# Optimization experiments

Hardware: AMD Instinct MI355X
Metric: run time of the kernel (lower is better)

Reference implementation:

```python
import jax, jax.numpy as jnp
import numpy as np

N = 50000   # nodes
D = 128     # hidden_dim == in_dim
H = 4       # heads
C = 32      # hidden_dim // heads
L = 3       # message_layers
ET = 640000 # temporal edges
EH = 320000 # host edges


def layer_norm(x, g, b, eps=1e-5):
    m = x.mean(-1, keepdims=True)
    v = ((x - m) ** 2).mean(-1, keepdims=True)
    return (x - m) / jnp.sqrt(v + eps) * g + b


def transformer_conv(h, src, dst, e_emb, Wq, bq, Wk, bk, Wv, bv, We, Ws, bs):
    # PyG TransformerConv, concat=True, root_weight=True, beta=False
    n = h.shape[0]
    q = (h @ Wq + bq).reshape(n, H, C)
    k = (h @ Wk + bk).reshape(n, H, C)
    v = (h @ Wv + bv).reshape(n, H, C)
    ee = (e_emb @ We).reshape(-1, H, C)          # lin_edge has no bias
    kj = k[src] + ee                              # [E,H,C]
    a = (q[dst] * kj).sum(-1) / np.sqrt(C)        # [E,H]
    amax = jax.ops.segment_max(a, dst, num_segments=n)
    amax = jnp.where(jnp.isfinite(amax), amax, 0.0)
    ex = jnp.exp(a - amax[dst])
    den = jax.ops.segment_sum(ex, dst, num_segments=n)
    alpha = ex / (den[dst] + 1e-16)               # segment softmax over in-edges of dst
    msg = (v[src] + ee) * alpha[..., None]        # [E,H,C]
    out = jax.ops.segment_sum(msg, dst, num_segments=n).reshape(n, H * C)
    return out + h @ Ws + bs                      # root/skip connection


def mlp_head(h, W1, b1, g, bt, W2, b2):
    z = jax.nn.silu(h @ W1 + b1)
    z = layer_norm(z, g, bt)
    return z @ W2 + b2


def setup_inputs() -> dict:
    key = jax.random.key(0)
    ks = iter(jax.random.split(key, 80))
    nrm = lambda shape: jax.random.normal(next(ks), shape, jnp.float32) * 0.05
    inp = {}
    inp['x'] = jax.random.normal(next(ks), (N, D), jnp.float32)
    inp['edge_index_temporal'] = jax.random.randint(next(ks), (2, ET), 0, N)
    inp['edge_index_host'] = jax.random.randint(next(ks), (2, EH), 0, N)
    inp['edge_attr_temporal'] = jax.random.uniform(next(ks), (ET, 1), jnp.float32)
    inp['edge_attr_host'] = jax.random.normal(next(ks), (EH, 3), jnp.float32)
    # edge encoders
    inp['W_tedge'] = nrm((1, 4)); inp['b_tedge'] = jnp.zeros(4)
    inp['W_hedge'] = nrm((3, 4)); inp['b_hedge'] = jnp.zeros(4)
    # stacked conv params [L, ...] for temporal (_t) and host (_h) convs
    for s in ('t', 'h'):
        inp[f'Wq_{s}'] = nrm((L, D, D)); inp[f'bq_{s}'] = jnp.zeros((L, D))
        inp[f'Wk_{s}'] = nrm((L, D, D)); inp[f'bk_{s}'] = jnp.zeros((L, D))
        inp[f'Wv_{s}'] = nrm((L, D, D)); inp[f'bv_{s}'] = jnp.zeros((L, D))
        inp[f'We_{s}'] = nrm((L, 4, D))
        inp[f'Ws_{s}'] = nrm((L, D, D)); inp[f'bs_{s}'] = jnp.zeros((L, D))
    inp['norm_g'] = jnp.ones((L, D)); inp['norm_b'] = jnp.zeros((L, D))
    inp['fg'] = jnp.ones(D); inp['fb'] = jnp.zeros(D)
    inp['dW1'] = nrm((D, D)); inp['db1'] = jnp.zeros(D)
    inp['dg'] = jnp.ones(D); inp['dbt'] = jnp.zeros(D)
    inp['dW2'] = nrm((D, 3)); inp['db2'] = jnp.zeros(3)
    inp['sW1'] = nrm((D, D)); inp['sb1'] = jnp.zeros(D)
    inp['sg'] = jnp.ones(D); inp['sbt'] = jnp.zeros(D)
    inp['sW2'] = nrm((D, 3)); inp['sb2'] = jnp.zeros(3)
    return inp


def reference(x, edge_index_temporal, edge_index_host, edge_attr_temporal, edge_attr_host,
              W_tedge, b_tedge, W_hedge, b_hedge,
              Wq_t, bq_t, Wk_t, bk_t, Wv_t, bv_t, We_t, Ws_t, bs_t,
              Wq_h, bq_h, Wk_h, bk_h, Wv_h, bv_h, We_h, Ws_h, bs_h,
              norm_g, norm_b, fg, fb,
              dW1, db1, dg, dbt, dW2, db2,
              sW1, sb1, sg, sbt, sW2, sb2):
    te = edge_attr_temporal @ W_tedge + b_tedge   # [ET, edge_dim]
    he = edge_attr_host @ W_hedge + b_hedge       # [EH, edge_dim]
    st, dt_ = edge_index_temporal[0], edge_index_temporal[1]
    sh, dh = edge_index_host[0], edge_index_host[1]
    h = x
    for l in range(L):
        t_out = transformer_conv(h, st, dt_, te, Wq_t[l], bq_t[l], Wk_t[l], bk_t[l],
                                 Wv_t[l], bv_t[l], We_t[l], Ws_t[l], bs_t[l])
        h_out = transformer_conv(h, sh, dh, he, Wq_h[l], bq_h[l], Wk_h[l], bk_h[l],
                                 Wv_h[l], bv_h[l], We_h[l], Ws_h[l], bs_h[l])
        combined = jax.nn.silu(layer_norm(t_out + h_out, norm_g[l], norm_b[l]))
        h = h + combined  # residual (shapes match since in_dim == hidden_dim)
    h = layer_norm(h, fg, fb)
    drift = mlp_head(h, dW1, db1, dg, dbt, dW2, db2)
    diff = mlp_head(h, sW1, sb1, sg, sbt, sW2, sb2)
    return drift, diff
```

## Files before the change

### kernel.cpp

```cpp
#include <hip/hip_runtime.h>
#include <math.h>

#define NN 50000
#define DD 128
#define ET_N 640000
#define EH_N 320000
#define NL 3

static inline int cdiv(int a, int b){ return (a+b-1)/b; }

typedef __attribute__((ext_vector_type(8))) short short8;
typedef __attribute__((ext_vector_type(4))) float f32x4;

__device__ float   g_h [(size_t)NN*DD];
__device__ unsigned short g_hb[(size_t)NN*DD];
__device__ unsigned short g_Wb[(size_t)NL*8*DD*DD];
__device__ float   g_Q [2][(size_t)NN*DD];
__device__ float   g_S [2][(size_t)NN*DD];
__device__ ushort2 g_KV[2][(size_t)NN*DD];
__device__ float   g_to[(size_t)NN*DD];
__device__ float   g_ho[(size_t)NN*DD];
__device__ int     g_cnt[2][NN];
__device__ int     g_cur[2][NN];
__device__ int     g_rs [2][NN+1];
__device__ int     g_srcc[2][ET_N];
__device__ float4  g_ee  [2][ET_N];

__device__ inline unsigned short f2bf(float f){
  unsigned u = __float_as_uint(f);
  unsigned r = (u + 0x7fffu + ((u>>16)&1u)) >> 16;
  return (unsigned short)r;
}
__device__ inline float bf2f(unsigned short s){
  return __uint_as_float(((unsigned)s)<<16);
}

__global__ void k_copy_h(const float* __restrict__ x){
  int i = blockIdx.x*256 + threadIdx.x;
  if (i < NN*DD/4){
    float4 v = reinterpret_cast<const float4*>(x)[i];
    reinterpret_cast<float4*>(g_h)[i] = v;
    ushort4 b; b.x=f2bf(v.x); b.y=f2bf(v.y); b.z=f2bf(v.z); b.w=f2bf(v.w);
    reinterpret_cast<ushort4*>(g_hb)[i] = b;
  }
}

__global__ void k_zero_cnt(){
  int i = blockIdx.x*256 + threadIdx.x;
  if (i < NN) g_cnt[blockIdx.y][i] = 0;
}

struct WPtrs { const float* W[24]; };
__global__ __launch_bounds__(256) void k_cvtw(WPtrs wp){
  int mat = blockIdx.y;
  const float* W = wp.W[mat];
  int e = blockIdx.x*256 + threadIdx.x;
  int n = e >> 7, k = e & 127;
  g_Wb[(size_t)mat*DD*DD + e] = f2bf(W[k*DD+n]);
}

__global__ void k_hist(const int* __restrict__ dstT, const int* __restrict__ dstH){
  int which = blockIdx.y;
  int E = which ? EH_N : ET_N;
  const int* dst = which ? dstH : dstT;
  int e = blockIdx.x*256+threadIdx.x;
  if (e<E) atomicAdd(&g_cnt[which][dst[e]], 1);
}

__global__ __launch_bounds__(1024) void k_scan(){
  int which = blockIdx.y;
  int* row_start = g_rs[which];
  const int* cnt = g_cnt[which];
  int* cur = g_cur[which];
  __shared__ int buf[1024];
  int tid = threadIdx.x;
  const int n = NN;
  int chunk = (n + 1023) >> 10;
  int start = tid*chunk; if (start>n) start=n;
  int end = start+chunk; if (end>n) end=n;
  int lsum=0;
  for (int i=start;i<end;++i) lsum += cnt[i];
  buf[tid]=lsum;
  __syncthreads();
  for (int off=1; off<1024; off<<=1){
    int t = (tid>=off)? buf[tid-off]:0;
    __syncthreads();
    buf[tid] += t;
    __syncthreads();
  }
  int run = buf[tid]-lsum;
  for (int i=start;i<end;++i){ row_start[i]=run; cur[i]=run; run += cnt[i]; }
  if (tid==1023) row_start[n]=run;
}

__global__ void k_scatter(const int* __restrict__ eit, const int* __restrict__ eih,
                          const float* __restrict__ attrT, const float* __restrict__ attrH,
                          const float* __restrict__ Wt, const float* __restrict__ bt4,
                          const float* __restrict__ Wh, const float* __restrict__ bh4){
  int which = blockIdx.y;
  int e = blockIdx.x*256+threadIdx.x;
  if (which==0){
    if (e>=ET_N) return;
    int src = eit[e], dst = eit[ET_N+e];
    int p = atomicAdd(&g_cur[0][dst],1);
    g_srcc[0][p]=src;
    float a = attrT[e];
    g_ee[0][p] = make_float4(a*Wt[0]+bt4[0], a*Wt[1]+bt4[1], a*Wt[2]+bt4[2], a*Wt[3]+bt4[3]);
  } else {
    if (e>=EH_N) return;
    int src = eih[e], dst = eih[EH_N+e];
    int p = atomicAdd(&g_cur[1][dst],1);
    g_srcc[1][p]=src;
    float a0=attrH[e*3+0], a1=attrH[e*3+1], a2=attrH[e*3+2];
    float4 v;
    v.x = a0*Wh[0]+a1*Wh[4]+a2*Wh[8]+bh4[0];
    v.y = a0*Wh[1]+a1*Wh[5]+a2*Wh[9]+bh4[1];
    v.z = a0*Wh[2]+a1*Wh[6]+a2*Wh[10]+bh4[2];
    v.w = a0*Wh[3]+a1*Wh[7]+a2*Wh[11]+bh4[3];
    g_ee[1][p] = v;
  }
}

struct BiasP { const float* b[8]; };

__global__ __launch_bounds__(256) void k_gemm_mfma(int l, BiasP bp){
  __shared__ unsigned short lA[64*DD];
  __shared__ unsigned short lB[DD*DD];
  int y = blockIdx.y;
  int conv = y/3, kind = y%3;
  int setbase = l*8 + conv*4;
  const unsigned short* Wm0 = &g_Wb[(size_t)(setbase + (kind==0?0:(kind==1?1:3)))*DD*DD];
  const unsigned short* Wm1 = &g_Wb[(size_t)(setbase+2)*DD*DD];
  int tid = threadIdx.x;
  int m0 = blockIdx.x*64;

#pragma unroll
  for (int p=0;p<4;++p){
    int c = tid + p*256;
    int row = c >> 4, col16 = c & 15;
    int grow = m0 + row;
    uint4 v = make_uint4(0,0,0,0);
    if (grow < NN) v = *reinterpret_cast<const uint4*>(&g_hb[(size_t)grow*DD + col16*8]);
    int off = (row*256 + col16*16) ^ ((row&7)<<4);
    *reinterpret_cast<uint4*>((char*)lA + off) = v;
  }
#pragma unroll
  for (int p=0;p<8;++p){
    int c = tid + p*256;
    int row = c >> 4, col16 = c & 15;
    uint4 v = *reinterpret_cast<const uint4*>(&Wm0[(size_t)row*DD + col16*8]);
    int off = (row*256 + col16*16) ^ ((row&7)<<4);
    *reinterpret_cast<uint4*>((char*)lB + off) = v;
  }
  __syncthreads();

  int wave = tid >> 6, lane = tid & 63;
  int lrow = lane & 15, kg = lane >> 4;
  int n0w = wave*32;

  short8 a[4][4];
#pragma unroll
  for (int kk=0;kk<4;++kk){
    int kbyte = kk*64 + kg*16;
#pragma unroll
    for (int mi=0;mi<4;++mi){
      int row = mi*16 + lrow;
      int off = (row*256 + kbyte) ^ ((row&7)<<4);
      a[kk][mi] = *reinterpret_cast<const short8*>((char*)lA + off);
    }
  }

  f32x4 acc[4][2];
#pragma unroll
  for (int mi=0;mi<4;++mi)
#pragma unroll
    for (int ni=0;ni<2;++ni) acc[mi][ni] = (f32x4){0.f,0.f,0.f,0.f};

#pragma unroll
  for (int kk=0;kk<4;++kk){
    int kbyte = kk*64 + kg*16;
    short8 b[2];
#pragma unroll
    for (int ni=0;ni<2;++ni){
      int n = n0w + ni*16 + lrow;
      int off = (n*256 + kbyte) ^ ((n&7)<<4);
      b[ni] = *reinterpret_cast<const short8*>((char*)lB + off);
    }
#pragma unroll
    for (int mi=0;mi<4;++mi)
#pragma unroll
      for (int ni=0;ni<2;++ni)
        acc[mi][ni] = __builtin_amdgcn_mfma_f32_16x16x32_bf16(a[kk][mi], b[ni], acc[mi][ni], 0,0,0);
  }

  f32x4 acc2[4][2];
  if (kind==1){
    __syncthreads();
#pragma unroll
    for (int p=0;p<8;++p){
      int c = tid + p*256;
      int row = c >> 4, col16 = c & 15;
      uint4 v = *reinterpret_cast<const uint4*>(&Wm1[(size_t)row*DD + col16*8]);
      int off = (row*256 + col16*16) ^ ((row&7)<<4);
      *reinterpret_cast<uint4*>((char*)lB + off) = v;
    }
    __syncthreads();
#pragma unroll
    for (int mi=0;mi<4;++mi)
#pragma unroll
      for (int ni=0;ni<2;++ni) acc2[mi][ni] = (f32x4){0.f,0.f,0.f,0.f};
#pragma unroll
    for (int kk=0;kk<4;++kk){
      int kbyte = kk*64 + kg*16;
      short8 b[2];
#pragma unroll
      for (int ni=0;ni<2;++ni){
        int n = n0w + ni*16 + lrow;
        int off = (n*256 + kbyte) ^ ((n&7)<<4);
        b[ni] = *reinterpret_cast<const short8*>((char*)lB + off);
      }
#pragma unroll
      for (int mi=0;mi<4;++mi)
#pragma unroll
        for (int ni=0;ni<2;++ni)
          acc2[mi][ni] = __builtin_amdgcn_mfma_f32_16x16x32_bf16(a[kk][mi], b[ni], acc2[mi][ni], 0,0,0);
    }
  }

  const float* bias0 = bp.b[conv*4 + (kind==0?0:(kind==1?1:3))];
  const float* bias1 = bp.b[conv*4 + 2];
#pragma unroll
  for (int ni=0;ni<2;++ni){
    int col = n0w + ni*16 + lrow;
    float bs0 = bias0[col];
    float bs1 = (kind==1) ? bias1[col] : 0.f;
#pragma unroll
    for (int mi=0;mi<4;++mi){
#pragma unroll
      for (int r=0;r<4;++r){
        int row = m0 + mi*16 + kg*4 + r;
        if (row >= NN) continue;
        size_t o = (size_t)row*DD + col;
        if (kind==1){
          ushort2 kv;
          kv.x = f2bf(acc[mi][ni][r]  + bs0);
          kv.y = f2bf(acc2[mi][ni][r] + bs1);
          g_KV[conv][o] = kv;
        } else {
          float* op = (kind==0) ? g_Q[conv] : g_S[conv];
          op[o] = acc[mi][ni][r] + bs0;
        }
      }
    }
  }
}

__global__ __launch_bounds__(128) void k_agg(const float* __restrict__ WeT,
                                             const float* __restrict__ WeH){
  int conv = blockIdx.y;
  int i = blockIdx.x;
  int d = threadIdx.x;
  const float* We = conv ? WeH : WeT;
  float w0=We[d], w1=We[DD+d], w2=We[2*DD+d], w3=We[3*DD+d];
  float qd = g_Q[conv][(size_t)i*DD+d];
  const int*     srcc = g_srcc[conv];
  const float4*  ee   = g_ee[conv];
  const ushort2* KV   = g_KV[conv];
  int beg=g_rs[conv][i], end=g_rs[conv][i+1];
  float m=-INFINITY, den=0.f, acc=0.f;
  if (beg<end){
    int s = srcc[beg];
    float4 e4 = ee[beg];
    ushort2 kv = KV[(size_t)s*DD+d];
    for (int idx=beg; idx<end; ++idx){
      ushort2 kv_n = kv; float4 e4_n = e4;
      if (idx+1<end){
        int s_n = srcc[idx+1];
        e4_n = ee[idx+1];
        kv_n = KV[(size_t)s_n*DD+d];
      }
      float eev = e4.x*w0 + e4.y*w1 + e4.z*w2 + e4.w*w3;
      float kf = bf2f(kv.x), vf = bf2f(kv.y);
      float p = qd*(kf+eev);
      p += __shfl_xor(p,16); p += __shfl_xor(p,8); p += __shfl_xor(p,4);
      p += __shfl_xor(p,2);  p += __shfl_xor(p,1);
      float a = p*0.17677669529663687f;
      float nm = fmaxf(m,a);
      float sc = __expf(m-nm);
      float ea = __expf(a-nm);
      den = den*sc + ea;
      acc = acc*sc + ea*(vf+eev);
      m = nm;
      kv = kv_n; e4 = e4_n;
    }
  }
  float r = acc/(den+1e-16f) + g_S[conv][(size_t)i*DD+d];
  float* o = conv ? g_ho : g_to;
  o[(size_t)i*DD+d] = r;
}

__device__ inline float waveRed(float v){
  v += __shfl_xor(v,32); v += __shfl_xor(v,16); v += __shfl_xor(v,8);
  v += __shfl_xor(v,4);  v += __shfl_xor(v,2);  v += __shfl_xor(v,1);
  return v;
}

__global__ __launch_bounds__(256) void k_combine(const float* __restrict__ g, const float* __restrict__ bt){
  int lane = threadIdx.x & 63;
  int node = blockIdx.x*4 + (threadIdx.x>>6);
  if (node>=NN) return;
  size_t i0 = (size_t)node*DD + lane, i1 = i0+64;
  float v0 = g_to[i0] + g_ho[i0];
  float v1 = g_to[i1] + g_ho[i1];
  float s = waveRed(v0+v1);
  float mean = s*(1.f/128.f);
  float d0=v0-mean, d1=v1-mean;
  float q = waveRed(d0*d0+d1*d1);
  float inv = 1.f/sqrtf(q*(1.f/128.f)+1e-5f);
  float c0 = d0*inv*g[lane]+bt[lane];
  float c1 = d1*inv*g[lane+64]+bt[lane+64];
  float h0 = g_h[i0] + c0/(1.f+expf(-c0));
  float h1 = g_h[i1] + c1/(1.f+expf(-c1));
  g_h[i0] = h0; g_h[i1] = h1;
  g_hb[i0] = f2bf(h0); g_hb[i1] = f2bf(h1);
}

__global__ __launch_bounds__(256) void k_finalln(const float* __restrict__ g, const float* __restrict__ b){
  int lane = threadIdx.x & 63;
  int node = blockIdx.x*4 + (threadIdx.x>>6);
  if (node>=NN) return;
  size_t i0 = (size_t)node*DD + lane, i1 = i0+64;
  float v0 = g_h[i0], v1 = g_h[i1];
  float s = waveRed(v0+v1);
  float mean = s*(1.f/128.f);
  float d0=v0-mean, d1=v1-mean;
  float q = waveRed(d0*d0+d1*d1);
  float inv = 1.f/sqrtf(q*(1.f/128.f)+1e-5f);
  g_h[i0]=d0*inv*g[lane]+b[lane];
  g_h[i1]=d1*inv*g[lane+64]+b[lane+64];
}

__global__ __launch_bounds__(128) void k_head(
      const float* __restrict__ W1, const float* __restrict__ b1,
      const float* __restrict__ g, const float* __restrict__ bt,
      const float* __restrict__ W2, const float* __restrict__ b2,
      float* __restrict__ out){
  int d = threadIdx.x;
  int wv = d >> 6;
  int i0 = blockIdx.x*8;
  const int n = NN;
  __shared__ float rows[8][DD];
  __shared__ float comb[2];
#pragma unroll
  for (int t=0;t<8;++t){
    int node = i0+t;
    rows[t][d] = (node<n)? g_h[(size_t)node*DD+d] : 0.f;
  }
  __syncthreads();
  float z[8];
  float b1d = b1[d];
#pragma unroll
  for (int t=0;t<8;++t) z[t]=b1d;
  for (int k=0;k<DD;++k){
    float w = W1[k*DD+d];
#pragma unroll
    for (int t=0;t<8;++t) z[t] += rows[t][k]*w;
  }
#pragma unroll
  for (int t=0;t<8;++t){ float v=z[t]; z[t] = v/(1.f+expf(-v)); }
  float gd=g[d], btd=bt[d];
  float w2a=W2[d*3+0], w2b=W2[d*3+1], w2c=W2[d*3+2];
  float b2a=b2[0], b2b=b2[1], b2c=b2[2];
  for (int t=0;t<8;++t){
    int node=i0+t;
    float zz=z[t];
    float s = waveRed(zz);
    if ((d&63)==0) comb[wv]=s;
    __syncthreads();
    float mean=(comb[0]+comb[1])*(1.f/128.f);
    __syncthreads();
    float dv=zz-mean;
    float q2 = waveRed(dv*dv);
    if ((d&63)==0) comb[wv]=q2;
    __syncthreads();
    float inv = 1.f/sqrtf((comb[0]+comb[1])*(1.f/128.f)+1e-5f);
    __syncthreads();
    float zn = dv*inv*gd+btd;
    float p0 = waveRed(zn*w2a);
    if ((d&63)==0) comb[wv]=p0;
    __syncthreads();
    float o0 = comb[0]+comb[1]+b2a;
    __syncthreads();
    float p1 = waveRed(zn*w2b);
    if ((d&63)==0) comb[wv]=p1;
    __syncthreads();
    float o1 = comb[0]+comb[1]+b2b;
    __syncthreads();
    float p2 = waveRed(zn*w2c);
    if ((d&63)==0) comb[wv]=p2;
    __syncthreads();
    float o2 = comb[0]+comb[1]+b2c;
    __syncthreads();
    if (d==0 && node<n){
      out[(size_t)node*3+0]=o0; out[(size_t)node*3+1]=o1; out[(size_t)node*3+2]=o2;
    }
  }
}

extern "C" void kernel_launch(void* const* d_in, const int* in_sizes, int n_in,
                              void* d_out, int out_size, void* d_ws, size_t ws_size,
                              hipStream_t stream){
  (void)in_sizes; (void)n_in; (void)out_size; (void)d_ws; (void)ws_size;
  const float* x    = (const float*)d_in[0];
  const int*   eit  = (const int*)d_in[1];
  const int*   eih  = (const int*)d_in[2];
  const float* eat  = (const float*)d_in[3];
  const float* eah  = (const float*)d_in[4];
  const float* W_te = (const float*)d_in[5];
  const float* b_te = (const float*)d_in[6];
  const float* W_he = (const float*)d_in[7];
  const float* b_he = (const float*)d_in[8];
  const float *Wq_t=(const float*)d_in[9],  *bq_t=(const float*)d_in[10];
  const float *Wk_t=(const float*)d_in[11], *bk_t=(const float*)d_in[12];
  const float *Wv_t=(const float*)d_in[13], *bv_t=(const float*)d_in[14];
  const float *We_t=(const float*)d_in[15];
  const float *Ws_t=(const float*)d_in[16], *bs_t=(const float*)d_in[17];
  const float *Wq_h=(const float*)d_in[18], *bq_h=(const float*)d_in[19];
  const float *Wk_h=(const float*)d_in[20], *bk_h=(const float*)d_in[21];
  const float *Wv_h=(const float*)d_in[22], *bv_h=(const float*)d_in[23];
  const float *We_h=(const float*)d_in[24];
  const float *Ws_h=(const float*)d_in[25], *bs_h=(const float*)d_in[26];
  const float *norm_g=(const float*)d_in[27], *norm_b=(const float*)d_in[28];
  const float *fg=(const float*)d_in[29], *fb=(const float*)d_in[30];
  const float *dW1=(const float*)d_in[31], *db1=(const float*)d_in[32];
  const float *dg=(const float*)d_in[33],  *dbt=(const float*)d_in[34];
  const float *dW2=(const float*)d_in[35], *db2=(const float*)d_in[36];
  const float *sW1=(const float*)d_in[37], *sb1=(const float*)d_in[38];
  const float *sg=(const float*)d_in[39],  *sbt=(const float*)d_in[40];
  const float *sW2=(const float*)d_in[41], *sb2=(const float*)d_in[42];
  float* outp = (float*)d_out;

  k_copy_h<<<cdiv(NN*DD/4,256),256,0,stream>>>(x);

  WPtrs wp;
  for (int l=0;l<NL;++l){
    wp.W[l*8+0]=Wq_t+(size_t)l*DD*DD; wp.W[l*8+1]=Wk_t+(size_t)l*DD*DD;
    wp.W[l*8+2]=Wv_t+(size_t)l*DD*DD; wp.W[l*8+3]=Ws_t+(size_t)l*DD*DD;
    wp.W[l*8+4]=Wq_h+(size_t)l*DD*DD; wp.W[l*8+5]=Wk_h+(size_t)l*DD*DD;
    wp.W[l*8+6]=Wv_h+(size_t)l*DD*DD; wp.W[l*8+7]=Ws_h+(size_t)l*DD*DD;
  }
  k_cvtw<<<dim3(64,24),256,0,stream>>>(wp);

  k_zero_cnt<<<dim3(cdiv(NN,256),2),256,0,stream>>>();
  k_hist<<<dim3(cdiv(ET_N,256),2),256,0,stream>>>(eit+ET_N, eih+EH_N);
  k_scan<<<dim3(1,2),1024,0,stream>>>();
  k_scatter<<<dim3(cdiv(ET_N,256),2),256,0,stream>>>(eit, eih, eat, eah, W_te, b_te, W_he, b_he);

  for (int l=0;l<NL;++l){
    BiasP bp;
    bp.b[0]=bq_t+(size_t)l*DD; bp.b[1]=bk_t+(size_t)l*DD;
    bp.b[2]=bv_t+(size_t)l*DD; bp.b[3]=bs_t+(size_t)l*DD;
    bp.b[4]=bq_h+(size_t)l*DD; bp.b[5]=bk_h+(size_t)l*DD;
    bp.b[6]=bv_h+(size_t)l*DD; bp.b[7]=bs_h+(size_t)l*DD;
    k_gemm_mfma<<<dim3(cdiv(NN,64),6),256,0,stream>>>(l, bp);
    k_agg<<<dim3(NN,2),128,0,stream>>>(We_t+(size_t)l*4*DD, We_h+(size_t)l*4*DD);
    k_combine<<<cdiv(NN,4),256,0,stream>>>(norm_g+(size_t)l*DD, norm_b+(size_t)l*DD);
  }
  k_finalln<<<cdiv(NN,4),256,0,stream>>>(fg, fb);
  k_head<<<cdiv(NN,8),128,0,stream>>>(dW1, db1, dg, dbt, dW2, db2, outp);
  k_head<<<cdiv(NN,8),128,0,stream>>>(sW1, sb1, sg, sbt, sW2, sb2, outp+(size_t)NN*3);
}
```

Before: 1.384 ms.

## Fold edge embeddings algebraically into aggregation, merge projection GEMMs, dual-stream softmax

Edge features are no longer expanded to 4-dim embeddings at scatter time. The raw attributes are stored instead, and the edge-embedding contribution is folded per node into precomputed q·(W_enc·We) head scalars and weighted-attribute accumulators. The aggregation loop processes two edges per iteration with two independent online-softmax streams that are merged at the end, which adds parallelism to hide gather latency. The GEMM kernel now computes all four projections per block, reusing the A tile, instead of using six separate block rows. The SiLU in the combine step switches to the fast exp. In exchange there are more registers in k_agg and the GEMM kernel has fewer blocks.

```diff
diff --git a/kernel.cpp b/kernel.cpp
--- a/kernel.cpp
+++ b/kernel.cpp
@@ -24,7 +24,8 @@
 __device__ int     g_cur[2][NN];
 __device__ int     g_rs [2][NN+1];
 __device__ int     g_srcc[2][ET_N];
-__device__ float4  g_ee  [2][ET_N];
+__device__ float   g_ta[ET_N];
+__device__ float4  g_ha[EH_N];
 
 __device__ inline unsigned short f2bf(float f){
   unsigned u = __float_as_uint(f);
@@ -94,9 +95,7 @@
 }
 
 __global__ void k_scatter(const int* __restrict__ eit, const int* __restrict__ eih,
-                          const float* __restrict__ attrT, const float* __restrict__ attrH,
-                          const float* __restrict__ Wt, const float* __restrict__ bt4,
-                          const float* __restrict__ Wh, const float* __restrict__ bh4){
+                          const float* __restrict__ attrT, const float* __restrict__ attrH){
   int which = blockIdx.y;
   int e = blockIdx.x*256+threadIdx.x;
   if (which==0){
@@ -104,20 +103,13 @@
     int src = eit[e], dst = eit[ET_N+e];
     int p = atomicAdd(&g_cur[0][dst],1);
     g_srcc[0][p]=src;
-    float a = attrT[e];
-    g_ee[0][p] = make_float4(a*Wt[0]+bt4[0], a*Wt[1]+bt4[1], a*Wt[2]+bt4[2], a*Wt[3]+bt4[3]);
+    g_ta[p]=attrT[e];
   } else {
     if (e>=EH_N) return;
     int src = eih[e], dst = eih[EH_N+e];
     int p = atomicAdd(&g_cur[1][dst],1);
     g_srcc[1][p]=src;
-    float a0=attrH[e*3+0], a1=attrH[e*3+1], a2=attrH[e*3+2];
-    float4 v;
-    v.x = a0*Wh[0]+a1*Wh[4]+a2*Wh[8]+bh4[0];
-    v.y = a0*Wh[1]+a1*Wh[5]+a2*Wh[9]+bh4[1];
-    v.z = a0*Wh[2]+a1*Wh[6]+a2*Wh[10]+bh4[2];
-    v.w = a0*Wh[3]+a1*Wh[7]+a2*Wh[11]+bh4[3];
-    g_ee[1][p] = v;
+    g_ha[p]=make_float4(attrH[e*3+0],attrH[e*3+1],attrH[e*3+2],0.f);
   }
 }
 
@@ -126,11 +118,8 @@
 __global__ __launch_bounds__(256) void k_gemm_mfma(int l, BiasP bp){
   __shared__ unsigned short lA[64*DD];
   __shared__ unsigned short lB[DD*DD];
-  int y = blockIdx.y;
-  int conv = y/3, kind = y%3;
+  int conv = blockIdx.y;
   int setbase = l*8 + conv*4;
-  const unsigned short* Wm0 = &g_Wb[(size_t)(setbase + (kind==0?0:(kind==1?1:3)))*DD*DD];
-  const unsigned short* Wm1 = &g_Wb[(size_t)(setbase+2)*DD*DD];
   int tid = threadIdx.x;
   int m0 = blockIdx.x*64;
 
@@ -144,19 +133,24 @@
     int off = (row*256 + col16*16) ^ ((row&7)<<4);
     *reinterpret_cast<uint4*>((char*)lA + off) = v;
   }
-#pragma unroll
-  for (int p=0;p<8;++p){
-    int c = tid + p*256;
-    int row = c >> 4, col16 = c & 15;
-    uint4 v = *reinterpret_cast<const uint4*>(&Wm0[(size_t)row*DD + col16*8]);
-    int off = (row*256 + col16*16) ^ ((row&7)<<4);
-    *reinterpret_cast<uint4*>((char*)lB + off) = v;
-  }
-  __syncthreads();
 
   int wave = tid >> 6, lane = tid & 63;
   int lrow = lane & 15, kg = lane >> 4;
   int n0w = wave*32;
+
+  auto stageB = [&](const unsigned short* Wm){
+#pragma unroll
+    for (int p=0;p<8;++p){
+      int c = tid + p*256;
+      int row = c >> 4, col16 = c & 15;
+      uint4 v = *reinterpret_cast<const uint4*>(&Wm[(size_t)row*DD + col16*8]);
+      int off = (row*256 + col16*16) ^ ((row&7)<<4);
+      *reinterpret_cast<uint4*>((char*)lB + off) = v;
+    }
+  };
+
+  stageB(&g_Wb[(size_t)(setbase+0)*DD*DD]);
+  __syncthreads();
 
   short8 a[4][4];
 #pragma unroll
@@ -170,45 +164,11 @@
     }
   }
 
-  f32x4 acc[4][2];
-#pragma unroll
-  for (int mi=0;mi<4;++mi)
-#pragma unroll
-    for (int ni=0;ni<2;++ni) acc[mi][ni] = (f32x4){0.f,0.f,0.f,0.f};
-
-#pragma unroll
-  for (int kk=0;kk<4;++kk){
-    int kbyte = kk*64 + kg*16;
-    short8 b[2];
-#pragma unroll
-    for (int ni=0;ni<2;++ni){
-      int n = n0w + ni*16 + lrow;
-      int off = (n*256 + kbyte) ^ ((n&7)<<4);
-      b[ni] = *reinterpret_cast<const short8*>((char*)lB + off);
-    }
+  auto computeC = [&](f32x4 (&acc)[4][2]){
 #pragma unroll
     for (int mi=0;mi<4;++mi)
 #pragma unroll
-      for (int ni=0;ni<2;++ni)
-        acc[mi][ni] = __builtin_amdgcn_mfma_f32_16x16x32_bf16(a[kk][mi], b[ni], acc[mi][ni], 0,0,0);
-  }
-
-  f32x4 acc2[4][2];
-  if (kind==1){
-    __syncthreads();
-#pragma unroll
-    for (int p=0;p<8;++p){
-      int c = tid + p*256;
-      int row = c >> 4, col16 = c & 15;
-      uint4 v = *reinterpret_cast<const uint4*>(&Wm1[(size_t)row*DD + col16*8]);
-      int off = (row*256 + col16*16) ^ ((row&7)<<4);
-      *reinterpret_cast<uint4*>((char*)lB + off) = v;
-    }
-    __syncthreads();
-#pragma unroll
-    for (int mi=0;mi<4;++mi)
-#pragma unroll
-      for (int ni=0;ni<2;++ni) acc2[mi][ni] = (f32x4){0.f,0.f,0.f,0.f};
+      for (int ni=0;ni<2;++ni) acc[mi][ni] = (f32x4){0.f,0.f,0.f,0.f};
 #pragma unroll
     for (int kk=0;kk<4;++kk){
       int kbyte = kk*64 + kg*16;
@@ -223,86 +183,211 @@
       for (int mi=0;mi<4;++mi)
 #pragma unroll
         for (int ni=0;ni<2;++ni)
-          acc2[mi][ni] = __builtin_amdgcn_mfma_f32_16x16x32_bf16(a[kk][mi], b[ni], acc2[mi][ni], 0,0,0);
-    }
-  }
-
-  const float* bias0 = bp.b[conv*4 + (kind==0?0:(kind==1?1:3))];
-  const float* bias1 = bp.b[conv*4 + 2];
-#pragma unroll
-  for (int ni=0;ni<2;++ni){
-    int col = n0w + ni*16 + lrow;
-    float bs0 = bias0[col];
-    float bs1 = (kind==1) ? bias1[col] : 0.f;
-#pragma unroll
-    for (int mi=0;mi<4;++mi){
-#pragma unroll
-      for (int r=0;r<4;++r){
-        int row = m0 + mi*16 + kg*4 + r;
-        if (row >= NN) continue;
-        size_t o = (size_t)row*DD + col;
-        if (kind==1){
-          ushort2 kv;
-          kv.x = f2bf(acc[mi][ni][r]  + bs0);
-          kv.y = f2bf(acc2[mi][ni][r] + bs1);
-          g_KV[conv][o] = kv;
-        } else {
-          float* op = (kind==0) ? g_Q[conv] : g_S[conv];
-          op[o] = acc[mi][ni][r] + bs0;
+          acc[mi][ni] = __builtin_amdgcn_mfma_f32_16x16x32_bf16(a[kk][mi], b[ni], acc[mi][ni], 0,0,0);
+    }
+  };
+
+  f32x4 acc[4][2], accK[4][2];
+
+  computeC(acc);
+  {
+    const float* bias = bp.b[conv*4+0];
+    float* op = g_Q[conv];
+#pragma unroll
+    for (int ni=0;ni<2;++ni){
+      int col = n0w + ni*16 + lrow;
+      float bs = bias[col];
+#pragma unroll
+      for (int mi=0;mi<4;++mi)
+#pragma unroll
+        for (int r=0;r<4;++r){
+          int row = m0 + mi*16 + kg*4 + r;
+          if (row < NN) op[(size_t)row*DD + col] = acc[mi][ni][r] + bs;
         }
-      }
-    }
-  }
-}
-
-__global__ __launch_bounds__(128) void k_agg(const float* __restrict__ WeT,
-                                             const float* __restrict__ WeH){
-  int conv = blockIdx.y;
-  int i = blockIdx.x;
-  int d = threadIdx.x;
-  const float* We = conv ? WeH : WeT;
-  float w0=We[d], w1=We[DD+d], w2=We[2*DD+d], w3=We[3*DD+d];
-  float qd = g_Q[conv][(size_t)i*DD+d];
-  const int*     srcc = g_srcc[conv];
-  const float4*  ee   = g_ee[conv];
-  const ushort2* KV   = g_KV[conv];
-  int beg=g_rs[conv][i], end=g_rs[conv][i+1];
-  float m=-INFINITY, den=0.f, acc=0.f;
-  if (beg<end){
-    int s = srcc[beg];
-    float4 e4 = ee[beg];
-    ushort2 kv = KV[(size_t)s*DD+d];
-    for (int idx=beg; idx<end; ++idx){
-      ushort2 kv_n = kv; float4 e4_n = e4;
-      if (idx+1<end){
-        int s_n = srcc[idx+1];
-        e4_n = ee[idx+1];
-        kv_n = KV[(size_t)s_n*DD+d];
-      }
-      float eev = e4.x*w0 + e4.y*w1 + e4.z*w2 + e4.w*w3;
-      float kf = bf2f(kv.x), vf = bf2f(kv.y);
-      float p = qd*(kf+eev);
-      p += __shfl_xor(p,16); p += __shfl_xor(p,8); p += __shfl_xor(p,4);
-      p += __shfl_xor(p,2);  p += __shfl_xor(p,1);
-      float a = p*0.17677669529663687f;
-      float nm = fmaxf(m,a);
-      float sc = __expf(m-nm);
-      float ea = __expf(a-nm);
-      den = den*sc + ea;
-      acc = acc*sc + ea*(vf+eev);
-      m = nm;
-      kv = kv_n; e4 = e4_n;
-    }
-  }
-  float r = acc/(den+1e-16f) + g_S[conv][(size_t)i*DD+d];
-  float* o = conv ? g_ho : g_to;
-  o[(size_t)i*DD+d] = r;
+    }
+  }
+  __syncthreads();
+  stageB(&g_Wb[(size_t)(setbase+1)*DD*DD]);
+  __syncthreads();
+  computeC(accK);
+  __syncthreads();
+  stageB(&g_Wb[(size_t)(setbase+2)*DD*DD]);
+  __syncthreads();
+  computeC(acc);
+  {
+    const float* bK = bp.b[conv*4+1];
+    const float* bV = bp.b[conv*4+2];
+#pragma unroll
+    for (int ni=0;ni<2;++ni){
+      int col = n0w + ni*16 + lrow;
+      float bk = bK[col], bv = bV[col];
+#pragma unroll
+      for (int mi=0;mi<4;++mi)
+#pragma unroll
+        for (int r=0;r<4;++r){
+          int row = m0 + mi*16 + kg*4 + r;
+          if (row < NN){
+            ushort2 kv;
+            kv.x = f2bf(accK[mi][ni][r] + bk);
+            kv.y = f2bf(acc [mi][ni][r] + bv);
+            g_KV[conv][(size_t)row*DD + col] = kv;
+          }
+        }
+    }
+  }
+  __syncthreads();
+  stageB(&g_Wb[(size_t)(setbase+3)*DD*DD]);
+  __syncthreads();
+  computeC(acc);
+  {
+    const float* bias = bp.b[conv*4+3];
+    float* op = g_S[conv];
+#pragma unroll
+    for (int ni=0;ni<2;++ni){
+      int col = n0w + ni*16 + lrow;
+      float bs = bias[col];
+#pragma unroll
+      for (int mi=0;mi<4;++mi)
+#pragma unroll
+        for (int r=0;r<4;++r){
+          int row = m0 + mi*16 + kg*4 + r;
+          if (row < NN) op[(size_t)row*DD + col] = acc[mi][ni][r] + bs;
+        }
+    }
+  }
 }
 
 __device__ inline float waveRed(float v){
   v += __shfl_xor(v,32); v += __shfl_xor(v,16); v += __shfl_xor(v,8);
   v += __shfl_xor(v,4);  v += __shfl_xor(v,2);  v += __shfl_xor(v,1);
   return v;
+}
+__device__ inline float headRed(float v){
+  v += __shfl_xor(v,16); v += __shfl_xor(v,8); v += __shfl_xor(v,4);
+  v += __shfl_xor(v,2);  v += __shfl_xor(v,1);
+  return v;
+}
+
+__global__ __launch_bounds__(128) void k_agg(
+    const float* __restrict__ WeT, const float* __restrict__ WeH,
+    const float* __restrict__ Wt,  const float* __restrict__ bt4,
+    const float* __restrict__ Wh,  const float* __restrict__ bh4){
+  int conv = blockIdx.y;
+  int i = blockIdx.x;
+  int d = threadIdx.x;
+
+  float c0=0.f,c1=0.f,c2=0.f,c3=0.f;
+  if (conv==0){
+#pragma unroll
+    for (int j=0;j<4;++j){ float w=WeT[j*DD+d]; c1 += Wt[j]*w; c0 += bt4[j]*w; }
+  } else {
+#pragma unroll
+    for (int j=0;j<4;++j){
+      float w=WeH[j*DD+d];
+      c0 += Wh[j]*w; c1 += Wh[4+j]*w; c2 += Wh[8+j]*w; c3 += bh4[j]*w;
+    }
+  }
+
+  float qd = g_Q[conv][(size_t)i*DD+d];
+  float qe0,qe1,qe2=0.f,qe3=0.f;
+  if (conv==0){
+    qe0 = headRed(qd*c0);
+    qe1 = headRed(qd*c1);
+  } else {
+    qe0 = headRed(qd*c0);
+    qe1 = headRed(qd*c1);
+    qe2 = headRed(qd*c2);
+    qe3 = headRed(qd*c3);
+  }
+
+  const int*     srcc = g_srcc[conv];
+  const ushort2* KV   = g_KV[conv];
+  int beg=g_rs[conv][i], end=g_rs[conv][i+1];
+  int cnt = end-beg;
+
+  const float inv32 = 0.17677669529663687f;
+  float mA=-INFINITY,dnA=0.f,acA=0.f,x0A=0.f,x1A=0.f,x2A=0.f;
+  float mB=-INFINITY,dnB=0.f,acB=0.f,x0B=0.f,x1B=0.f,x2B=0.f;
+
+  if (cnt>0){
+    ushort2 kv0=make_ushort2(0,0), kv1=make_ushort2(0,0);
+    float4 a0v=make_float4(0.f,0.f,0.f,0.f), a1v=a0v;
+    bool h1;
+    {
+      int s0=srcc[beg];
+      if (conv==0) a0v.x=g_ta[beg]; else a0v=g_ha[beg];
+      kv0=KV[(size_t)s0*DD+d];
+      h1 = (beg+1<end);
+      if (h1){
+        int s1=srcc[beg+1];
+        if (conv==0) a1v.x=g_ta[beg+1]; else a1v=g_ha[beg+1];
+        kv1=KV[(size_t)s1*DD+d];
+      }
+    }
+    for (int t=beg; t<end; t+=2){
+      ushort2 ckv0=kv0, ckv1=kv1; float4 ca0=a0v, ca1=a1v; bool ch1=h1;
+      int tn=t+2;
+      if (tn<end){
+        int s0=srcc[tn];
+        if (conv==0) a0v.x=g_ta[tn]; else a0v=g_ha[tn];
+        kv0=KV[(size_t)s0*DD+d];
+        h1 = (tn+1<end);
+        if (h1){
+          int s1=srcc[tn+1];
+          if (conv==0) a1v.x=g_ta[tn+1]; else a1v=g_ha[tn+1];
+          kv1=KV[(size_t)s1*DD+d];
+        }
+      }
+      float p0 = qd*bf2f(ckv0.x);
+      float p1 = ch1 ? qd*bf2f(ckv1.x) : 0.f;
+#pragma unroll
+      for (int mk=16; mk>=1; mk>>=1){ p0 += __shfl_xor(p0,mk); p1 += __shfl_xor(p1,mk); }
+      float lg0, lg1;
+      if (conv==0){
+        lg0 = (p0 + qe0 + ca0.x*qe1)*inv32;
+        lg1 = (p1 + qe0 + ca1.x*qe1)*inv32;
+      } else {
+        lg0 = (p0 + ca0.x*qe0 + ca0.y*qe1 + ca0.z*qe2 + qe3)*inv32;
+        lg1 = (p1 + ca1.x*qe0 + ca1.y*qe1 + ca1.z*qe2 + qe3)*inv32;
+      }
+      {
+        float nm=fmaxf(mA,lg0), sc=__expf(mA-nm), ea=__expf(lg0-nm);
+        dnA=dnA*sc+ea; acA=acA*sc+ea*bf2f(ckv0.y);
+        x0A=x0A*sc+ea*ca0.x;
+        if (conv==1){ x1A=x1A*sc+ea*ca0.y; x2A=x2A*sc+ea*ca0.z; }
+        mA=nm;
+      }
+      if (ch1){
+        float nm=fmaxf(mB,lg1), sc=__expf(mB-nm), ea=__expf(lg1-nm);
+        dnB=dnB*sc+ea; acB=acB*sc+ea*bf2f(ckv1.y);
+        x0B=x0B*sc+ea*ca1.x;
+        if (conv==1){ x1B=x1B*sc+ea*ca1.y; x2B=x2B*sc+ea*ca1.z; }
+        mB=nm;
+      }
+    }
+  }
+
+  float r;
+  if (cnt==0){
+    r = 0.f;
+  } else {
+    float mm = fmaxf(mA,mB);
+    float eA = __expf(mA-mm), eB = __expf(mB-mm);
+    float den = dnA*eA + dnB*eB;
+    float ac  = acA*eA + acB*eB;
+    float x0  = x0A*eA + x0B*eB;
+    float id = 1.f/den;
+    if (conv==0){
+      r = ac*id + c0 + c1*(x0*id);
+    } else {
+      float x1 = x1A*eA + x1B*eB;
+      float x2 = x2A*eA + x2B*eB;
+      r = ac*id + c0*(x0*id) + c1*(x1*id) + c2*(x2*id) + c3;
+    }
+  }
+  r += g_S[conv][(size_t)i*DD+d];
+  float* o = conv ? g_ho : g_to;
+  o[(size_t)i*DD+d] = r;
 }
 
 __global__ __launch_bounds__(256) void k_combine(const float* __restrict__ g, const float* __restrict__ bt){
@@ -319,8 +404,8 @@
   float inv = 1.f/sqrtf(q*(1.f/128.f)+1e-5f);
   float c0 = d0*inv*g[lane]+bt[lane];
   float c1 = d1*inv*g[lane+64]+bt[lane+64];
-  float h0 = g_h[i0] + c0/(1.f+expf(-c0));
-  float h1 = g_h[i1] + c1/(1.f+expf(-c1));
+  float h0 = g_h[i0] + c0/(1.f+__expf(-c0));
+  float h1 = g_h[i1] + c1/(1.f+__expf(-c1));
   g_h[i0] = h0; g_h[i1] = h1;
   g_hb[i0] = f2bf(h0); g_hb[i1] = f2bf(h1);
 }
@@ -454,7 +539,7 @@
   k_zero_cnt<<<dim3(cdiv(NN,256),2),256,0,stream>>>();
   k_hist<<<dim3(cdiv(ET_N,256),2),256,0,stream>>>(eit+ET_N, eih+EH_N);
   k_scan<<<dim3(1,2),1024,0,stream>>>();
-  k_scatter<<<dim3(cdiv(ET_N,256),2),256,0,stream>>>(eit, eih, eat, eah, W_te, b_te, W_he, b_he);
+  k_scatter<<<dim3(cdiv(ET_N,256),2),256,0,stream>>>(eit, eih, eat, eah);
 
   for (int l=0;l<NL;++l){
     BiasP bp;
@@ -462,8 +547,9 @@
     bp.b[2]=bv_t+(size_t)l*DD; bp.b[3]=bs_t+(size_t)l*DD;
     bp.b[4]=bq_h+(size_t)l*DD; bp.b[5]=bk_h+(size_t)l*DD;
     bp.b[6]=bv_h+(size_t)l*DD; bp.b[7]=bs_h+(size_t)l*DD;
-    k_gemm_mfma<<<dim3(cdiv(NN,64),6),256,0,stream>>>(l, bp);
-    k_agg<<<dim3(NN,2),128,0,stream>>>(We_t+(size_t)l*4*DD, We_h+(size_t)l*4*DD);
+    k_gemm_mfma<<<dim3(cdiv(NN,64),2),256,0,stream>>>(l, bp);
+    k_agg<<<dim3(NN,2),128,0,stream>>>(We_t+(size_t)l*4*DD, We_h+(size_t)l*4*DD,
+                                       W_te, b_te, W_he, b_he);
     k_combine<<<cdiv(NN,4),256,0,stream>>>(norm_g+(size_t)l*DD, norm_b+(size_t)l*DD);
   }
   k_finalln<<<cdiv(NN,4),256,0,stream>>>(fg, fb);
```

Result: faster. 1.318 ms (-4.8%).
